# Optimization experiments

Hardware: AMD Instinct MI355X
Metric: run time of the kernel (lower is better)

## Reference

```python
import jax, jax.numpy as jnp
import numpy as np

N_PTS = 4_194_304   # query points per iteration
N_TREES = 64        # number of occupied forest blocks
RES = 64            # occupancy grid resolution per block
L = 8               # block lookup table side (8x8x8 possible block slots)


def setup_inputs() -> dict:
    key = jax.random.key(0)
    k1, k2, k3 = jax.random.split(key, 3)
    # World coords in [0, L); world_origin = 0, world_block_size = 1.
    pts = jax.random.uniform(k1, (N_PTS, 3), dtype=jnp.float32) * L
    # EMA occupancy values per block, [n_trees, res, res, res].
    occ_val_grid = jax.random.uniform(k2, (N_TREES, RES, RES, RES), dtype=jnp.float32)
    # Sparse forest: only N_TREES of the L^3 block slots hold a block; rest map to -1.
    perm = jax.random.permutation(k3, L * L * L)
    lookup = -jnp.ones((L * L * L,), dtype=jnp.int32)
    lookup = lookup.at[perm[:N_TREES]].set(jnp.arange(N_TREES, dtype=jnp.int32))
    block_lookup = lookup.reshape(L, L, L)
    return {"pts": pts, "occ_val_grid": occ_val_grid, "block_lookup": block_lookup}


def reference(pts, occ_val_grid, block_lookup):
    # query_world: normalize_coords -> block lookup -> per-voxel occupancy gather.
    L = block_lookup.shape[0]
    res = occ_val_grid.shape[1]
    # Which block each point falls in (world_origin=0, world_block_size=1).
    bc = jnp.floor(pts).astype(jnp.int32)                       # [N,3]
    in_dom = jnp.all((bc >= 0) & (bc < L), axis=-1)             # [N]
    bcs = jnp.clip(bc, 0, L - 1)
    bidx = block_lookup[bcs[:, 0], bcs[:, 1], bcs[:, 2]]        # [N], -1 = no block
    bidx = jnp.where(in_dom, bidx, -1)
    # [-1,1] normalized in-block coords.
    block_x = 2.0 * (pts - bcs.astype(pts.dtype)) - 1.0
    # Voxel indices within the block's occupancy grid.
    vox = jnp.clip(jnp.floor((block_x * 0.5 + 0.5) * res), 0, res - 1).astype(jnp.int32)
    valid = bidx >= 0
    safe_bidx = jnp.where(valid, bidx, 0)
    vals = occ_val_grid[safe_bidx, vox[:, 0], vox[:, 1], vox[:, 2]]  # irregular gather
    # Points outside the forest are unoccupied (occ value 0).
    return jnp.where(valid, vals, jnp.zeros((), dtype=vals.dtype))
```

## Files before the change

### kernel.cpp

```cpp
#include <hip/hip_runtime.h>


#define LDIM 8
#define RES  64

typedef float v4f __attribute__((ext_vector_type(4)));

__device__ __forceinline__ void compute_idx4(
    const int* __restrict__ slut, v4f q0, v4f q1, v4f q2,
    int idx[4], bool valid[4])
{
    const float xs[4] = {q0.x, q0.w, q1.z, q2.y};
    const float ys[4] = {q0.y, q1.x, q1.w, q2.z};
    const float zs[4] = {q0.z, q1.y, q2.x, q2.w};
#pragma unroll
    for (int k = 0; k < 4; ++k) {
        float x = xs[k], y = ys[k], z = zs[k];

        int bx = (int)floorf(x);
        int by = (int)floorf(y);
        int bz = (int)floorf(z);
        bool in_dom = (bx >= 0) & (bx < LDIM) &
                      (by >= 0) & (by < LDIM) &
                      (bz >= 0) & (bz < LDIM);
        int cx = min(max(bx, 0), LDIM - 1);
        int cy = min(max(by, 0), LDIM - 1);
        int cz = min(max(bz, 0), LDIM - 1);

        int bidx = slut[(cx * LDIM + cy) * LDIM + cz];
        bool v = in_dom & (bidx >= 0);

        float bxf = 2.0f * (x - (float)cx) - 1.0f;
        float byf = 2.0f * (y - (float)cy) - 1.0f;
        float bzf = 2.0f * (z - (float)cz) - 1.0f;
        float tx = (bxf * 0.5f + 0.5f) * (float)RES;
        float ty = (byf * 0.5f + 0.5f) * (float)RES;
        float tz = (bzf * 0.5f + 0.5f) * (float)RES;
        int vx = min(max((int)floorf(tx), 0), RES - 1);
        int vy = min(max((int)floorf(ty), 0), RES - 1);
        int vz = min(max((int)floorf(tz), 0), RES - 1);

        int sb = v ? bidx : 0;
        int ii = ((sb * RES + vx) * RES + vy) * RES + vz;
        idx[k]   = v ? ii : 0;
        valid[k] = v;
    }
}

__global__ __launch_bounds__(256, 8) void occ_forest_kernel(
    const v4f*    __restrict__ pts4,
    const float*  __restrict__ grid,
    const int*    __restrict__ lookup,
    v4f*          __restrict__ out4,
    int T)
{
    __shared__ int slut[LDIM * LDIM * LDIM];

    {
        const int2* lk2 = (const int2*)lookup;
        ((int2*)slut)[threadIdx.x] = lk2[threadIdx.x];
    }
    __syncthreads();

    int j = blockIdx.x * blockDim.x + threadIdx.x;

    const v4f* pA = pts4 + 3 * j;
    v4f a0 = __builtin_nontemporal_load(pA + 0);
    v4f a1 = __builtin_nontemporal_load(pA + 1);
    v4f a2 = __builtin_nontemporal_load(pA + 2);
    const v4f* pB = pts4 + 3 * (j + T);
    v4f b0 = __builtin_nontemporal_load(pB + 0);
    v4f b1 = __builtin_nontemporal_load(pB + 1);
    v4f b2 = __builtin_nontemporal_load(pB + 2);

    int  idxA[4];  bool valA[4];
    compute_idx4(slut, a0, a1, a2, idxA, valA);

    float vA[4];
#pragma unroll
    for (int k = 0; k < 4; ++k) vA[k] = grid[idxA[k]];

    int  idxB[4];  bool valB[4];
    compute_idx4(slut, b0, b1, b2, idxB, valB);

    float vB[4];
#pragma unroll
    for (int k = 0; k < 4; ++k) vB[k] = grid[idxB[k]];

#pragma unroll
    for (int k = 0; k < 4; ++k) vA[k] = valA[k] ? vA[k] : 0.0f;
    v4f oA = {vA[0], vA[1], vA[2], vA[3]};
    __builtin_nontemporal_store(oA, out4 + j);

#pragma unroll
    for (int k = 0; k < 4; ++k) vB[k] = valB[k] ? vB[k] : 0.0f;
    v4f oB = {vB[0], vB[1], vB[2], vB[3]};
    __builtin_nontemporal_store(oB, out4 + j + T);
}

extern "C" void kernel_launch(void* const* d_in, const int* in_sizes, int n_in,
                              void* d_out, int out_size, void* d_ws, size_t ws_size,
                              hipStream_t stream) {
    const float* pts    = (const float*)d_in[0];
    const float* grid   = (const float*)d_in[1];
    const int*   lookup = (const int*)d_in[2];
    float*       out    = (float*)d_out;

    int T = out_size / 8;
    int threads = 256;
    int blocks = (T + threads - 1) / threads;
    occ_forest_kernel<<<blocks, threads, 0, stream>>>(
        (const v4f*)pts, grid, lookup, (v4f*)out, T);
}
```

Before: 135.3 us.

## Split fused kernel into index-computation and gather kernels via output buffer

Splits the single fused kernel into two launches. The first computes flat grid indices from the points and writes them into the output buffer. The second reads those indices, gathers the occupancy values in place and writes them back. The aim is to separate streaming point reads from random grid gathers so each kernel has simpler access patterns and higher occupancy. In exchange it adds a second launch and an extra round trip of the index array through memory, and it drops the two-points-per-thread processing and the nontemporal hints.

```diff
diff --git a/kernel.cpp b/kernel.cpp
--- a/kernel.cpp
+++ b/kernel.cpp
@@ -5,14 +5,30 @@
 #define RES  64
 
 typedef float v4f __attribute__((ext_vector_type(4)));
+typedef int   v4i __attribute__((ext_vector_type(4)));
 
-__device__ __forceinline__ void compute_idx4(
-    const int* __restrict__ slut, v4f q0, v4f q1, v4f q2,
-    int idx[4], bool valid[4])
+__global__ __launch_bounds__(256) void idx_kernel(
+    const v4f* __restrict__ pts4,
+    const int* __restrict__ lookup,
+    v4i*       __restrict__ oidx,
+    int T)
 {
+    __shared__ int slut[LDIM * LDIM * LDIM];
+    ((int2*)slut)[threadIdx.x] = ((const int2*)lookup)[threadIdx.x];
+    __syncthreads();
+
+    int j = blockIdx.x * blockDim.x + threadIdx.x;
+
+    const v4f* p = pts4 + 3 * j;
+    v4f q0 = p[0];
+    v4f q1 = p[1];
+    v4f q2 = p[2];
+
     const float xs[4] = {q0.x, q0.w, q1.z, q2.y};
     const float ys[4] = {q0.y, q1.x, q1.w, q2.z};
     const float zs[4] = {q0.z, q1.y, q2.x, q2.w};
+
+    int idx[4];
 #pragma unroll
     for (int k = 0; k < 4; ++k) {
         float x = xs[k], y = ys[k], z = zs[k];
@@ -40,62 +56,36 @@
         int vy = min(max((int)floorf(ty), 0), RES - 1);
         int vz = min(max((int)floorf(tz), 0), RES - 1);
 
-        int sb = v ? bidx : 0;
-        int ii = ((sb * RES + vx) * RES + vy) * RES + vz;
-        idx[k]   = v ? ii : 0;
-        valid[k] = v;
+        int ii = ((bidx * RES + vx) * RES + vy) * RES + vz;
+        idx[k] = v ? ii : -1;
     }
+
+    v4i o = {idx[0], idx[1], idx[2], idx[3]};
+    oidx[j] = o;
 }
 
-__global__ __launch_bounds__(256, 8) void occ_forest_kernel(
-    const v4f*    __restrict__ pts4,
-    const float*  __restrict__ grid,
-    const int*    __restrict__ lookup,
-    v4f*          __restrict__ out4,
+__global__ __launch_bounds__(256) void gather_kernel(
+    const float* __restrict__ grid,
+    v4i*         __restrict__ io,
     int T)
 {
-    __shared__ int slut[LDIM * LDIM * LDIM];
-
-    {
-        const int2* lk2 = (const int2*)lookup;
-        ((int2*)slut)[threadIdx.x] = lk2[threadIdx.x];
-    }
-    __syncthreads();
-
     int j = blockIdx.x * blockDim.x + threadIdx.x;
 
-    const v4f* pA = pts4 + 3 * j;
-    v4f a0 = __builtin_nontemporal_load(pA + 0);
-    v4f a1 = __builtin_nontemporal_load(pA + 1);
-    v4f a2 = __builtin_nontemporal_load(pA + 2);
-    const v4f* pB = pts4 + 3 * (j + T);
-    v4f b0 = __builtin_nontemporal_load(pB + 0);
-    v4f b1 = __builtin_nontemporal_load(pB + 1);
-    v4f b2 = __builtin_nontemporal_load(pB + 2);
+    v4i idx = io[j];
 
-    int  idxA[4];  bool valA[4];
-    compute_idx4(slut, a0, a1, a2, idxA, valA);
+    float vals[4];
+#pragma unroll
+    for (int k = 0; k < 4; ++k) {
+        int i = idx[k];
+        vals[k] = grid[i < 0 ? 0 : i];
+    }
 
-    float vA[4];
+    v4i o;
 #pragma unroll
-    for (int k = 0; k < 4; ++k) vA[k] = grid[idxA[k]];
-
-    int  idxB[4];  bool valB[4];
-    compute_idx4(slut, b0, b1, b2, idxB, valB);
-
-    float vB[4];
-#pragma unroll
-    for (int k = 0; k < 4; ++k) vB[k] = grid[idxB[k]];
-
-#pragma unroll
-    for (int k = 0; k < 4; ++k) vA[k] = valA[k] ? vA[k] : 0.0f;
-    v4f oA = {vA[0], vA[1], vA[2], vA[3]};
-    __builtin_nontemporal_store(oA, out4 + j);
-
-#pragma unroll
-    for (int k = 0; k < 4; ++k) vB[k] = valB[k] ? vB[k] : 0.0f;
-    v4f oB = {vB[0], vB[1], vB[2], vB[3]};
-    __builtin_nontemporal_store(oB, out4 + j + T);
+    for (int k = 0; k < 4; ++k) {
+        o[k] = __float_as_int(idx[k] < 0 ? 0.0f : vals[k]);
+    }
+    io[j] = o;
 }
 
 extern "C" void kernel_launch(void* const* d_in, const int* in_sizes, int n_in,
@@ -104,11 +94,13 @@
     const float* pts    = (const float*)d_in[0];
     const float* grid   = (const float*)d_in[1];
     const int*   lookup = (const int*)d_in[2];
-    float*       out    = (float*)d_out;
 
-    int T = out_size / 8;
+    int T = out_size / 4;
     int threads = 256;
     int blocks = (T + threads - 1) / threads;
-    occ_forest_kernel<<<blocks, threads, 0, stream>>>(
-        (const v4f*)pts, grid, lookup, (v4f*)out, T);
+
+    idx_kernel<<<blocks, threads, 0, stream>>>(
+        (const v4f*)pts, lookup, (v4i*)d_out, T);
+    gather_kernel<<<blocks, threads, 0, stream>>>(
+        grid, (v4i*)d_out, T);
 }
```

Result: slower. 143.1 us (+5.8%).

## Process four point-quads per thread with 128-thread blocks and plain loads

Applied to the files above, without the earlier changes.

Each thread now handles four groups of four points instead of two, the block size drops to 128 threads, and the grid shrinks to match. The point-load order is changed so later groups load while earlier gathers are in flight. Nontemporal loads and stores are swapped for regular cached accesses. The LUT copy to shared memory uses int4 so 128 threads still fill it. The aim is more memory-level parallelism per thread and less per-block overhead, at the cost of more registers, fewer resident waves, and possible cache pollution from the cached streaming accesses.

```diff
diff --git a/kernel.cpp b/kernel.cpp
--- a/kernel.cpp
+++ b/kernel.cpp
@@ -5,6 +5,7 @@
 #define RES  64
 
 typedef float v4f __attribute__((ext_vector_type(4)));
+typedef int   v4i __attribute__((ext_vector_type(4)));
 
 __device__ __forceinline__ void compute_idx4(
     const int* __restrict__ slut, v4f q0, v4f q1, v4f q2,
@@ -47,7 +48,7 @@
     }
 }
 
-__global__ __launch_bounds__(256, 8) void occ_forest_kernel(
+__global__ __launch_bounds__(128, 4) void occ_forest_kernel(
     const v4f*    __restrict__ pts4,
     const float*  __restrict__ grid,
     const int*    __restrict__ lookup,
@@ -56,46 +57,65 @@
 {
     __shared__ int slut[LDIM * LDIM * LDIM];
 
-    {
-        const int2* lk2 = (const int2*)lookup;
-        ((int2*)slut)[threadIdx.x] = lk2[threadIdx.x];
-    }
+    ((v4i*)slut)[threadIdx.x] = ((const v4i*)lookup)[threadIdx.x];
     __syncthreads();
 
     int j = blockIdx.x * blockDim.x + threadIdx.x;
 
-    const v4f* pA = pts4 + 3 * j;
-    v4f a0 = __builtin_nontemporal_load(pA + 0);
-    v4f a1 = __builtin_nontemporal_load(pA + 1);
-    v4f a2 = __builtin_nontemporal_load(pA + 2);
-    const v4f* pB = pts4 + 3 * (j + T);
-    v4f b0 = __builtin_nontemporal_load(pB + 0);
-    v4f b1 = __builtin_nontemporal_load(pB + 1);
-    v4f b2 = __builtin_nontemporal_load(pB + 2);
+    const v4f* pA = pts4 + 3 * (j + 0 * T);
+    v4f a0 = pA[0], a1 = pA[1], a2 = pA[2];
+    const v4f* pB = pts4 + 3 * (j + 1 * T);
+    v4f b0 = pB[0], b1 = pB[1], b2 = pB[2];
 
-    int  idxA[4];  bool valA[4];
+    const v4f* pC = pts4 + 3 * (j + 2 * T);
+    v4f c0 = pC[0], c1 = pC[1], c2 = pC[2];
+
+    int idxA[4]; bool valA[4];
     compute_idx4(slut, a0, a1, a2, idxA, valA);
-
     float vA[4];
 #pragma unroll
     for (int k = 0; k < 4; ++k) vA[k] = grid[idxA[k]];
 
-    int  idxB[4];  bool valB[4];
+    const v4f* pD = pts4 + 3 * (j + 3 * T);
+    v4f d0 = pD[0], d1 = pD[1], d2 = pD[2];
+
+    int idxB[4]; bool valB[4];
     compute_idx4(slut, b0, b1, b2, idxB, valB);
-
     float vB[4];
 #pragma unroll
     for (int k = 0; k < 4; ++k) vB[k] = grid[idxB[k]];
 
+    int idxC[4]; bool valC[4];
+    compute_idx4(slut, c0, c1, c2, idxC, valC);
+    float vC[4];
+#pragma unroll
+    for (int k = 0; k < 4; ++k) vC[k] = grid[idxC[k]];
+
+    int idxD[4]; bool valD[4];
+    compute_idx4(slut, d0, d1, d2, idxD, valD);
+    float vD[4];
+#pragma unroll
+    for (int k = 0; k < 4; ++k) vD[k] = grid[idxD[k]];
+
 #pragma unroll
     for (int k = 0; k < 4; ++k) vA[k] = valA[k] ? vA[k] : 0.0f;
     v4f oA = {vA[0], vA[1], vA[2], vA[3]};
-    __builtin_nontemporal_store(oA, out4 + j);
+    out4[j + 0 * T] = oA;
 
 #pragma unroll
     for (int k = 0; k < 4; ++k) vB[k] = valB[k] ? vB[k] : 0.0f;
     v4f oB = {vB[0], vB[1], vB[2], vB[3]};
-    __builtin_nontemporal_store(oB, out4 + j + T);
+    out4[j + 1 * T] = oB;
+
+#pragma unroll
+    for (int k = 0; k < 4; ++k) vC[k] = valC[k] ? vC[k] : 0.0f;
+    v4f oC = {vC[0], vC[1], vC[2], vC[3]};
+    out4[j + 2 * T] = oC;
+
+#pragma unroll
+    for (int k = 0; k < 4; ++k) vD[k] = valD[k] ? vD[k] : 0.0f;
+    v4f oD = {vD[0], vD[1], vD[2], vD[3]};
+    out4[j + 3 * T] = oD;
 }
 
 extern "C" void kernel_launch(void* const* d_in, const int* in_sizes, int n_in,
@@ -106,8 +126,8 @@
     const int*   lookup = (const int*)d_in[2];
     float*       out    = (float*)d_out;
 
-    int T = out_size / 8;
-    int threads = 256;
+    int T = out_size / 16;
+    int threads = 128;
     int blocks = (T + threads - 1) / threads;
     occ_forest_kernel<<<blocks, threads, 0, stream>>>(
         (const v4f*)pts, grid, lookup, (v4f*)out, T);
```

New measurement: 138.6 us. +2.4%, slower.

## Bin valid points by tree and gather per tree in a second kernel

Applied to the files above, without the earlier changes.

The single fused gather kernel becomes a two-phase scheme. Phase 1 writes zeros for every point, stages valid (output index, grid index) pairs per tree in shared memory, then appends them to per-tree global buckets using one global atomic per tree per block. Phase 2 walks each tree's bucket and scatters the gathered grid values into the output. The aim is better cache locality for grid reads by grouping them per block. The cost is an extra memset, a second launch, bucket write and read traffic, and uncoalesced 4-byte scattered output writes.

```diff
diff --git a/kernel.cpp b/kernel.cpp
--- a/kernel.cpp
+++ b/kernel.cpp
@@ -3,12 +3,16 @@
 
 #define LDIM 8
 #define RES  64
+#define NTREE 64
+#define MAXPT 12288
+#define CNT_STRIDE 16
+#define STAGE_CAP 16
 
 typedef float v4f __attribute__((ext_vector_type(4)));
 
-__device__ __forceinline__ void compute_idx4(
+__device__ __forceinline__ void compute4(
     const int* __restrict__ slut, v4f q0, v4f q1, v4f q2,
-    int idx[4], bool valid[4])
+    int ii[4], int tr[4], bool valid[4])
 {
     const float xs[4] = {q0.x, q0.w, q1.z, q2.y};
     const float ys[4] = {q0.y, q1.x, q1.w, q2.z};
@@ -16,7 +20,6 @@
 #pragma unroll
     for (int k = 0; k < 4; ++k) {
         float x = xs[k], y = ys[k], z = zs[k];
-
         int bx = (int)floorf(x);
         int by = (int)floorf(y);
         int bz = (int)floorf(z);
@@ -41,28 +44,33 @@
         int vz = min(max((int)floorf(tz), 0), RES - 1);
 
         int sb = v ? bidx : 0;
-        int ii = ((sb * RES + vx) * RES + vy) * RES + vz;
-        idx[k]   = v ? ii : 0;
+        ii[k] = ((sb * RES + vx) * RES + vy) * RES + vz;
+        tr[k] = sb;
         valid[k] = v;
     }
 }
 
-__global__ __launch_bounds__(256, 8) void occ_forest_kernel(
-    const v4f*    __restrict__ pts4,
-    const float*  __restrict__ grid,
-    const int*    __restrict__ lookup,
-    v4f*          __restrict__ out4,
+__global__ __launch_bounds__(256) void phase1_kernel(
+    const v4f*   __restrict__ pts4,
+    const float* __restrict__ grid,
+    const int*   __restrict__ lookup,
+    v4f*         __restrict__ out4,
+    float*       __restrict__ out,
+    int*         __restrict__ counters,
+    int2*        __restrict__ entries,
     int T)
 {
-    __shared__ int slut[LDIM * LDIM * LDIM];
-
-    {
-        const int2* lk2 = (const int2*)lookup;
-        ((int2*)slut)[threadIdx.x] = lk2[threadIdx.x];
-    }
-    __syncthreads();
-
-    int j = blockIdx.x * blockDim.x + threadIdx.x;
+    __shared__ int  slut[LDIM * LDIM * LDIM];
+    __shared__ int  lcnt[NTREE];
+    __shared__ int  gbase[NTREE];
+    __shared__ int2 staged[NTREE * STAGE_CAP];
+
+    ((int2*)slut)[threadIdx.x] = ((const int2*)lookup)[threadIdx.x];
+    if (threadIdx.x < NTREE) lcnt[threadIdx.x] = 0;
+    __syncthreads();
+
+    int tid = threadIdx.x;
+    int j = blockIdx.x * blockDim.x + tid;
 
     const v4f* pA = pts4 + 3 * j;
     v4f a0 = __builtin_nontemporal_load(pA + 0);
@@ -73,28 +81,105 @@
     v4f b1 = __builtin_nontemporal_load(pB + 1);
     v4f b2 = __builtin_nontemporal_load(pB + 2);
 
-    int  idxA[4];  bool valA[4];
-    compute_idx4(slut, a0, a1, a2, idxA, valA);
-
-    float vA[4];
-#pragma unroll
-    for (int k = 0; k < 4; ++k) vA[k] = grid[idxA[k]];
-
-    int  idxB[4];  bool valB[4];
-    compute_idx4(slut, b0, b1, b2, idxB, valB);
-
-    float vB[4];
-#pragma unroll
-    for (int k = 0; k < 4; ++k) vB[k] = grid[idxB[k]];
-
-#pragma unroll
-    for (int k = 0; k < 4; ++k) vA[k] = valA[k] ? vA[k] : 0.0f;
-    v4f oA = {vA[0], vA[1], vA[2], vA[3]};
+    {
+        int ii[4], tr[4]; bool vv[4];
+        compute4(slut, a0, a1, a2, ii, tr, vv);
+        v4f oz = {0.0f, 0.0f, 0.0f, 0.0f};
+#pragma unroll
+        for (int k = 0; k < 4; ++k) {
+            if (vv[k]) {
+                int lp = atomicAdd(&lcnt[tr[k]], 1);
+                if (lp < STAGE_CAP) staged[tr[k] * STAGE_CAP + lp] = make_int2(4 * j + k, ii[k]);
+                else oz[k] = grid[ii[k]];
+            }
+        }
+        out4[j] = oz;
+    }
+    {
+        int ii[4], tr[4]; bool vv[4];
+        compute4(slut, b0, b1, b2, ii, tr, vv);
+        v4f oz = {0.0f, 0.0f, 0.0f, 0.0f};
+#pragma unroll
+        for (int k = 0; k < 4; ++k) {
+            if (vv[k]) {
+                int lp = atomicAdd(&lcnt[tr[k]], 1);
+                if (lp < STAGE_CAP) staged[tr[k] * STAGE_CAP + lp] = make_int2(4 * (j + T) + k, ii[k]);
+                else oz[k] = grid[ii[k]];
+            }
+        }
+        out4[j + T] = oz;
+    }
+    __syncthreads();
+
+    if (tid < NTREE) {
+        int c = lcnt[tid];
+        gbase[tid] = (c > 0) ? atomicAdd(&counters[tid * CNT_STRIDE], c) : 0;
+    }
+    __syncthreads();
+
+    {
+        int b = tid & 63;
+        int c = min(lcnt[b], STAGE_CAP);
+        for (int s = tid >> 6; s < c; s += 4) {
+            int g = gbase[b] + s;
+            int2 e = staged[b * STAGE_CAP + s];
+            if (g < MAXPT) entries[b * MAXPT + g] = e;
+            else out[e.x] = grid[e.y];
+        }
+    }
+}
+
+__global__ __launch_bounds__(256) void phase2_kernel(
+    const float* __restrict__ grid,
+    const int*   __restrict__ counters,
+    const int2*  __restrict__ entries,
+    float*       __restrict__ out)
+{
+    int t = blockIdx.x & 63;
+    int w = blockIdx.x >> 6;
+    int cnt = counters[t * CNT_STRIDE];
+    if (cnt > MAXPT) cnt = MAXPT;
+    const int2* eb = entries + t * MAXPT;
+    for (int i = w * 256 + (int)threadIdx.x; i < cnt; i += 16 * 256) {
+        int2 e = eb[i];
+        out[e.x] = grid[e.y];
+    }
+}
+
+__global__ __launch_bounds__(256, 8) void occ_forest_fallback(
+    const v4f* __restrict__ pts4, const float* __restrict__ grid,
+    const int* __restrict__ lookup, v4f* __restrict__ out4, int T)
+{
+    __shared__ int slut[LDIM * LDIM * LDIM];
+    ((int2*)slut)[threadIdx.x] = ((const int2*)lookup)[threadIdx.x];
+    __syncthreads();
+    int j = blockIdx.x * blockDim.x + threadIdx.x;
+    const v4f* pA = pts4 + 3 * j;
+    v4f a0 = __builtin_nontemporal_load(pA + 0);
+    v4f a1 = __builtin_nontemporal_load(pA + 1);
+    v4f a2 = __builtin_nontemporal_load(pA + 2);
+    const v4f* pB = pts4 + 3 * (j + T);
+    v4f b0 = __builtin_nontemporal_load(pB + 0);
+    v4f b1 = __builtin_nontemporal_load(pB + 1);
+    v4f b2 = __builtin_nontemporal_load(pB + 2);
+
+    int iiA[4], trA[4]; bool vA[4];
+    compute4(slut, a0, a1, a2, iiA, trA, vA);
+    float gA[4];
+#pragma unroll
+    for (int k = 0; k < 4; ++k) gA[k] = grid[vA[k] ? iiA[k] : 0];
+    int iiB[4], trB[4]; bool vB[4];
+    compute4(slut, b0, b1, b2, iiB, trB, vB);
+    float gB[4];
+#pragma unroll
+    for (int k = 0; k < 4; ++k) gB[k] = grid[vB[k] ? iiB[k] : 0];
+
+    v4f oA, oB;
+#pragma unroll
+    for (int k = 0; k < 4; ++k) oA[k] = vA[k] ? gA[k] : 0.0f;
+#pragma unroll
+    for (int k = 0; k < 4; ++k) oB[k] = vB[k] ? gB[k] : 0.0f;
     __builtin_nontemporal_store(oA, out4 + j);
-
-#pragma unroll
-    for (int k = 0; k < 4; ++k) vB[k] = valB[k] ? vB[k] : 0.0f;
-    v4f oB = {vB[0], vB[1], vB[2], vB[3]};
     __builtin_nontemporal_store(oB, out4 + j + T);
 }
 
@@ -104,11 +189,26 @@
     const float* pts    = (const float*)d_in[0];
     const float* grid   = (const float*)d_in[1];
     const int*   lookup = (const int*)d_in[2];
-    float*       out    = (float*)d_out;
 
     int T = out_size / 8;
     int threads = 256;
-    int blocks = (T + threads - 1) / threads;
-    occ_forest_kernel<<<blocks, threads, 0, stream>>>(
-        (const v4f*)pts, grid, lookup, (v4f*)out, T);
-}
+    int blocks = T / threads;
+
+    size_t cnt_bytes = (size_t)NTREE * CNT_STRIDE * sizeof(int);
+    size_t ent_bytes = (size_t)NTREE * MAXPT * sizeof(int2);
+    size_t need = cnt_bytes + ent_bytes;
+
+    if (ws_size >= need && d_ws != nullptr) {
+        int*  counters = (int*)d_ws;
+        int2* entries  = (int2*)((char*)d_ws + cnt_bytes);
+        hipMemsetAsync(d_ws, 0, cnt_bytes, stream);
+        phase1_kernel<<<blocks, threads, 0, stream>>>(
+            (const v4f*)pts, grid, lookup,
+            (v4f*)d_out, (float*)d_out, counters, entries, T);
+        phase2_kernel<<<1024, threads, 0, stream>>>(
+            grid, counters, entries, (float*)d_out);
+    } else {
+        occ_forest_fallback<<<blocks, threads, 0, stream>>>(
+            (const v4f*)pts, grid, lookup, (v4f*)d_out, T);
+    }
+}
```

Measured after the change: 183.0 us. 1.35x slower.
